# Performance work log

Hardware: AMD Instinct MI355X
Metric: run time of the kernel (lower is better)

## Reference

```python
import jax, jax.numpy as jnp
import numpy as np

NUM_TEAMS = 200000
EMBED_DIM = 16
NUM_EDGES = 3200000
BATCH = 500000
EPS_NORM = 1e-12  # F.normalize clamp
EPS_SOFTMAX = 1e-16  # PyG edge-softmax denom eps
NEG_SLOPE = 0.01  # LeakyReLU default


def setup_inputs() -> dict:
    key = jax.random.key(0)
    ks = jax.random.split(key, 12)
    inp = {}
    inp["embed"] = jax.random.normal(ks[0], (NUM_TEAMS, EMBED_DIM), dtype=jnp.float32)
    inp["beta"] = jnp.ones((2,), dtype=jnp.float32)  # one learnable scalar per AGNNConv
    # torch Linear init ~ U(-1/sqrt(fan_in), 1/sqrt(fan_in)); stored as [in, out]
    def lin(k, fi, fo):
        b = 1.0 / np.sqrt(fi)
        k1, k2 = jax.random.split(k)
        return (jax.random.uniform(k1, (fi, fo), jnp.float32, -b, b),
                jax.random.uniform(k2, (fo,), jnp.float32, -b, b))
    inp["lin0_w"], inp["lin0_b"] = lin(ks[1], 2 * EMBED_DIM, 6)
    inp["lin1_w"], inp["lin1_b"] = lin(ks[2], 6, 16)
    inp["lin2_w"], inp["lin2_b"] = lin(ks[3], 16, 3)
    inp["edge_index"] = jax.random.randint(ks[4], (2, NUM_EDGES), 0, NUM_TEAMS, dtype=jnp.int64)
    inp["home"] = jax.random.randint(ks[5], (BATCH,), 0, NUM_TEAMS, dtype=jnp.int64)
    inp["away"] = jax.random.randint(ks[6], (BATCH,), 0, NUM_TEAMS, dtype=jnp.int64)
    return inp


def _agnn_conv(x, beta, src, dst, n):
    # x: [N, D]; messages flow src(j) -> dst(i); scatter-softmax over edges per dst
    xn = x / jnp.maximum(jnp.linalg.norm(x, axis=-1, keepdims=True), EPS_NORM)
    alpha = beta * jnp.sum(xn[src] * xn[dst], axis=-1)          # [E]
    m = jax.ops.segment_max(alpha, dst, num_segments=n)          # [N]
    a = jnp.exp(alpha - m[dst])                                   # [E]
    denom = jax.ops.segment_sum(a, dst, num_segments=n)          # [N]
    a = a / (denom[dst] + EPS_SOFTMAX)
    return jax.ops.segment_sum(a[:, None] * x[src], dst, num_segments=n)  # [N, D]


def _forward(embed, beta, lin0_w, lin0_b, lin1_w, lin1_b, lin2_w, lin2_b,
             src, dst, home, away):
    n = embed.shape[0]
    act = lambda v: jax.nn.leaky_relu(v, NEG_SLOPE)
    x = embed  # embedding of arange(n_teams) == the table itself
    x = act(_agnn_conv(x, beta[0], src, dst, n))
    x = act(_agnn_conv(x, beta[1], src, dst, n))
    h = jnp.concatenate([x[home], x[away]], axis=-1)  # [B, 2D]
    h = act(h @ lin0_w + lin0_b)
    h = act(h @ lin1_w + lin1_b)
    h = act(h @ lin2_w + lin2_b)
    return jax.nn.log_softmax(h, axis=0).reshape(-1, 3)  # LogSoftmax(dim=0), faithful


def reference(embed, beta, lin0_w, lin0_b, lin1_w, lin1_b, lin2_w, lin2_b,
              edge_index, home, away):
    n = embed.shape[0]
    # AGNNConv default: remove then add self-loops
    loops = jnp.arange(n, dtype=edge_index.dtype)
    mask = edge_index[0] != edge_index[1]
    safe = jnp.where(mask, edge_index[1], edge_index[0])  # self-loop-out non-loop edges
    src = jnp.concatenate([edge_index[0], loops])
    dst = jnp.concatenate([jnp.where(mask, edge_index[1], edge_index[0]), loops])
    # masked self-loops in original list become src==dst duplicates of the appended
    # self-loops only if random collision; to faithfully *remove* them we redirect
    # removed edges onto the node's own appended self-loop (alpha identical for
    # src==dst), which changes only duplicate self-loop counts with prob ~1/N.
    return _forward(embed, beta, lin0_w, lin0_b, lin1_w, lin1_b, lin2_w, lin2_b,
                    src, dst, home, away)
```

## Files before the change

kernel.cpp:

```cpp
#include <hip/hip_runtime.h>
#include <hip/hip_fp16.h>
#include <math.h>

#define TPB 256
#define NPB 512
#define NPB_SHIFT 9
#define EPB 8192
#define EPW 16
#define BCAP 12288

typedef float v2f __attribute__((ext_vector_type(2)));

__device__ __forceinline__ float leaky_relu(float v) { return v > 0.0f ? v : 0.01f * v; }

__device__ __forceinline__ float dot4(float4 a, float4 b) {
    return a.x * b.x + a.y * b.y + a.z * b.z + a.w * b.w;
}
__device__ __forceinline__ float4 f4_scale(float4 a, float s) {
    return make_float4(a.x * s, a.y * s, a.z * s, a.w * s);
}
__device__ __forceinline__ float4 f4_acc(float4 a, float w, float4 y) {
    return make_float4(fmaf(w, y.x, a.x), fmaf(w, y.y, a.y),
                       fmaf(w, y.z, a.z), fmaf(w, y.w, a.w));
}
__device__ __forceinline__ float4 f4_add_shfl(float4 v, int d) {
    return make_float4(v.x + __shfl_xor(v.x, d, 64), v.y + __shfl_xor(v.y, d, 64),
                       v.z + __shfl_xor(v.z, d, 64), v.w + __shfl_xor(v.w, d, 64));
}
__device__ __forceinline__ float4 leaky4(float4 v) {
    return make_float4(leaky_relu(v.x), leaky_relu(v.y), leaky_relu(v.z), leaky_relu(v.w));
}

__device__ __forceinline__ float4 dec4(unsigned w) {
    v2f lo = __builtin_amdgcn_cvt_pk_f32_fp8((int)w, false);
    v2f hi = __builtin_amdgcn_cvt_pk_f32_fp8((int)w, true);
    return make_float4(lo.x, lo.y, hi.x, hi.y);
}
__device__ __forceinline__ unsigned enc4(float4 v) {
    int r = __builtin_amdgcn_cvt_pk_fp8_f32(v.x, v.y, 0, false);
    r = __builtin_amdgcn_cvt_pk_fp8_f32(v.z, v.w, r, true);
    return (unsigned)r;
}

__device__ __forceinline__ void store_h4(__half* row, int l, float4 v) {
    union { float2 f; __half h[4]; } u;
    u.h[0] = __float2half(v.x); u.h[1] = __float2half(v.y);
    u.h[2] = __float2half(v.z); u.h[3] = __float2half(v.w);
    ((float2*)row)[l] = u.f;
}

__device__ __forceinline__ int wave_incl_scan(int v, int lane) {
#pragma unroll
    for (int off = 1; off < 64; off <<= 1) {
        int u = __shfl_up(v, off, 64);
        if (lane >= off) v += u;
    }
    return v;
}

__global__ void k_binA(const int* __restrict__ src, const int* __restrict__ dst,
                       unsigned* __restrict__ bdata, int* __restrict__ cbase,
                       int* __restrict__ ccnt, int E, int K,
                       const float* __restrict__ x, uint4* __restrict__ xq,
                       int N) {
    __shared__ int hist[512];
    __shared__ unsigned lcol[EPB];
    __shared__ int wsum[8];
    int t = threadIdx.x;
    int lane = t & 63, wv = t >> 6;
    int c = blockIdx.x;
    int e0 = c * EPB;
    int e1 = min(e0 + EPB, E);
    int tot = e1 - e0;
    hist[t] = 0;
    __syncthreads();
    int myd[EPW], mys[EPW];
    if (tot == EPB) {
        const int4* d4 = (const int4*)(dst + e0);
        const int4* s4 = (const int4*)(src + e0);
#pragma unroll
        for (int k = 0; k < 4; ++k) {
            int4 dd = d4[t + k * 512];
            int4 ss = s4[t + k * 512];
            myd[4 * k + 0] = dd.x; myd[4 * k + 1] = dd.y;
            myd[4 * k + 2] = dd.z; myd[4 * k + 3] = dd.w;
            mys[4 * k + 0] = ss.x; mys[4 * k + 1] = ss.y;
            mys[4 * k + 2] = ss.z; mys[4 * k + 3] = ss.w;
            atomicAdd(&hist[dd.x >> NPB_SHIFT], 1);
            atomicAdd(&hist[dd.y >> NPB_SHIFT], 1);
            atomicAdd(&hist[dd.z >> NPB_SHIFT], 1);
            atomicAdd(&hist[dd.w >> NPB_SHIFT], 1);
        }
    } else {
#pragma unroll
        for (int k = 0; k < EPW; ++k) {
            int e = e0 + t + k * 512;
            int d = (e < e1) ? dst[e] : -1;
            mys[k] = (e < e1) ? src[e] : 0;
            myd[k] = d;
            if (d >= 0) atomicAdd(&hist[d >> NPB_SHIFT], 1);
        }
    }
    __syncthreads();
    int v = hist[t];
    int inc = wave_incl_scan(v, lane);
    if (lane == 63) wsum[wv] = inc;
    __syncthreads();
    if (t == 0) {
        int acc = 0;
#pragma unroll
        for (int k = 0; k < 8; ++k) { int xv = wsum[k]; wsum[k] = acc; acc += xv; }
    }
    __syncthreads();
    int excl = inc + wsum[wv] - v;
    if (t < K) {
        cbase[(size_t)c * K + t] = excl;
        ccnt[(size_t)c * K + t] = v;
    }
    __syncthreads();
    hist[t] = excl;
    __syncthreads();
    if (tot == EPB) {
#pragma unroll
        for (int k = 0; k < EPW; ++k) {
            int d = myd[k];
            int p = atomicAdd(&hist[d >> NPB_SHIFT], 1);
            lcol[p] = ((unsigned)(d & (NPB - 1)) << 18) | (unsigned)mys[k];
        }
    } else {
#pragma unroll
        for (int k = 0; k < EPW; ++k) {
            int d = myd[k];
            if (d >= 0) {
                int p = atomicAdd(&hist[d >> NPB_SHIFT], 1);
                lcol[p] = ((unsigned)(d & (NPB - 1)) << 18) | (unsigned)mys[k];
            }
        }
    }
    __syncthreads();
    unsigned* outp = bdata + (size_t)c * EPB;
    for (int i = t; i < tot; i += 512) outp[i] = lcol[i];
    int i = c * 512 + t;
    if (i < N) {
        const float4* xp = (const float4*)(x + (size_t)i * 16);
        float4 a = xp[0], b = xp[1], cc = xp[2], d = xp[3];
        xq[i] = make_uint4(enc4(a), enc4(b), enc4(cc), enc4(d));
    }
}

__global__ void k_binB(const unsigned* __restrict__ bdata, const int* __restrict__ cbase,
                       const int* __restrict__ ccnt,
                       int2* __restrict__ rng,
                       int* __restrict__ col, int N, int NC, int K) {
    __shared__ int cb[512];
    __shared__ int cc[512];
    __shared__ int ldeg[NPB];
    __shared__ int wsum[8];
    int b = blockIdx.x, t = threadIdx.x;
    int lane = t & 63, wv = t >> 6;
    int n0 = b << NPB_SHIFT;
    int nn = min(NPB, N - n0);
    cb[t] = (t < NC) ? cbase[(size_t)t * K + b] : 0;
    cc[t] = (t < NC) ? ccnt[(size_t)t * K + b] : 0;
    ldeg[t] = 0;
    __syncthreads();
    int mycnt = (t < NC) ? cc[t] : 0;
    const unsigned* myp = bdata + (size_t)t * EPB + cb[t];
    for (int k = 0; k < mycnt; ++k) {
        unsigned e = myp[k];
        atomicAdd(&ldeg[e >> 18], 1);
    }
    __syncthreads();
    int dv = ldeg[t];
    int inc = wave_incl_scan(dv, lane);
    if (lane == 63) wsum[wv] = inc;
    __syncthreads();
    if (t == 0) {
        int acc = 0;
#pragma unroll
        for (int k = 0; k < 8; ++k) { int xv = wsum[k]; wsum[k] = acc; acc += xv; }
    }
    __syncthreads();
    int excl = inc + wsum[wv] - dv;
    int gb = b * BCAP;
    if (t < nn) {
        rng[n0 + t] = make_int2(gb + excl, gb + excl + dv);
    }
    __syncthreads();
    ldeg[t] = excl;
    __syncthreads();
    for (int k = 0; k < mycnt; ++k) {
        unsigned e = myp[k];
        int pos = atomicAdd(&ldeg[e >> 18], 1);
        col[gb + pos] = (int)(e & 0x3FFFFu);
    }
}

__global__ void k_agnn(const uint4* __restrict__ xq,
                       const int2* __restrict__ rng,
                       const int* __restrict__ col,
                       const float* __restrict__ beta_ptr, int beta_idx,
                       void* __restrict__ out, int n, int fp8_out) {
    int t = threadIdx.x;
    int l = t & 7;
    int i = blockIdx.x * (512 / 8) + (t >> 3);
    if (i >= n) return;
    float bet = beta_ptr[beta_idx];
    uint4 rowi = xq[i];
    float4 x0 = dec4(rowi.x), x1 = dec4(rowi.y), x2 = dec4(rowi.z), x3 = dec4(rowi.w);
    float sqi = dot4(x0, x0) + dot4(x1, x1) + dot4(x2, x2) + dot4(x3, x3);
    float inv_ni = rsqrtf(fmaxf(sqi, 1e-24f));
    float bi = bet * inv_ni;
    float4 q0 = f4_scale(x0, bi), q1 = f4_scale(x1, bi),
           q2 = f4_scale(x2, bi), q3 = f4_scale(x3, bi);
    float s;
    float4 a0, a1, a2, a3;
    if (l == 0) {
        float w = __expf(bet);
        s = w;
        a0 = f4_scale(x0, w); a1 = f4_scale(x1, w);
        a2 = f4_scale(x2, w); a3 = f4_scale(x3, w);
    } else {
        s = 0.0f;
        a0 = a1 = a2 = a3 = make_float4(0.f, 0.f, 0.f, 0.f);
    }
    int2 se = rng[i];
    int e1 = se.y;
    int last = max(e1 - 1, 0);
    int e = se.x + l;
    int j0 = min(max(col[min(e, last)], 0), n - 1);
    uint4 rA = xq[j0];
    int j1 = min(max(col[min(e + 8, last)], 0), n - 1);
    uint4 rB = xq[j1];
    for (; e < e1; e += 8) {
        int j2 = min(max(col[min(e + 16, last)], 0), n - 1);
        uint4 rC = xq[j2];
        float4 y0 = dec4(rA.x), y1 = dec4(rA.y), y2 = dec4(rA.z), y3 = dec4(rA.w);
        float sq = dot4(y0, y0) + dot4(y1, y1) + dot4(y2, y2) + dot4(y3, y3);
        float inv_n = rsqrtf(fmaxf(sq, 1e-24f));
        float d = (dot4(y0, q0) + dot4(y1, q1) + dot4(y2, q2) + dot4(y3, q3)) * inv_n;
        float w = __expf(d);
        s += w;
        a0 = f4_acc(a0, w, y0);
        a1 = f4_acc(a1, w, y1);
        a2 = f4_acc(a2, w, y2);
        a3 = f4_acc(a3, w, y3);
        rA = rB; rB = rC;
    }
#pragma unroll
    for (int d_ = 1; d_ < 8; d_ <<= 1) {
        s += __shfl_xor(s, d_, 64);
        a0 = f4_add_shfl(a0, d_);
        a1 = f4_add_shfl(a1, d_);
        a2 = f4_add_shfl(a2, d_);
        a3 = f4_add_shfl(a3, d_);
    }
    float inv = 1.0f / (s + 1e-16f);
    float4 o0 = leaky4(f4_scale(a0, inv));
    float4 o1 = leaky4(f4_scale(a1, inv));
    float4 o2 = leaky4(f4_scale(a2, inv));
    float4 o3 = leaky4(f4_scale(a3, inv));
    if (l < 4) {
        float4 oq = (l == 0) ? o0 : (l == 1) ? o1 : (l == 2) ? o2 : o3;
        if (fp8_out) {
            ((unsigned*)((uint4*)out + i))[l] = enc4(oq);
        } else {
            store_h4((__half*)out + (size_t)i * 16, l, oq);
        }
    }
}

__global__ void k_mlp(const __half* __restrict__ x, const int* __restrict__ home,
                      const int* __restrict__ away,
                      const float* __restrict__ w0, const float* __restrict__ b0,
                      const float* __restrict__ w1, const float* __restrict__ b1,
                      const float* __restrict__ w2, const float* __restrict__ b2,
                      float* __restrict__ z, float* __restrict__ bmax,
                      float* __restrict__ bsum, int nb) {
    __shared__ float sw0[192], sw1[96], sw2[48], sb0[6], sb1[16], sb2[3];
    __shared__ float rmax[4][3];
    __shared__ float rsum[4][3];
    int t = threadIdx.x;
    if (t < 192) sw0[t] = w0[t];
    if (t < 96)  sw1[t] = w1[t];
    if (t < 48)  sw2[t] = w2[t];
    if (t < 6)   sb0[t] = b0[t];
    if (t < 16)  sb1[t] = b1[t];
    if (t < 3)   sb2[t] = b2[t];
    __syncthreads();
    int i = blockIdx.x * blockDim.x + t;
    bool act = i < nb;
    float z0 = -3.4e38f, z1 = -3.4e38f, z2 = -3.4e38f;
    if (act) {
        float h[32];
        const uint4* hr = (const uint4*)(x + (size_t)home[i] * 16);
        const uint4* ar = (const uint4*)(x + (size_t)away[i] * 16);
        uint4 hv0 = hr[0], hv1 = hr[1];
        uint4 av0 = ar[0], av1 = ar[1];
        union { uint4 u; __half2 h2[4]; } cv;
#pragma unroll
        for (int q = 0; q < 4; ++q) {
            cv.u = (q == 0) ? hv0 : (q == 1) ? hv1 : (q == 2) ? av0 : av1;
#pragma unroll
            for (int k = 0; k < 4; ++k) {
                float2 f = __half22float2(cv.h2[k]);
                h[q * 8 + 2 * k + 0] = f.x;
                h[q * 8 + 2 * k + 1] = f.y;
            }
        }
        float t0[6];
#pragma unroll
        for (int o = 0; o < 6; ++o) {
            float acc = sb0[o];
#pragma unroll
            for (int k = 0; k < 32; ++k) acc = fmaf(h[k], sw0[k * 6 + o], acc);
            t0[o] = leaky_relu(acc);
        }
        float t1[16];
#pragma unroll
        for (int o = 0; o < 16; ++o) {
            float acc = sb1[o];
#pragma unroll
            for (int k = 0; k < 6; ++k) acc = fmaf(t0[k], sw1[k * 16 + o], acc);
            t1[o] = leaky_relu(acc);
        }
        float zz[3];
#pragma unroll
        for (int o = 0; o < 3; ++o) {
            float acc = sb2[o];
#pragma unroll
            for (int k = 0; k < 16; ++k) acc = fmaf(t1[k], sw2[k * 3 + o], acc);
            zz[o] = leaky_relu(acc);
            z[(size_t)i * 3 + o] = zz[o];
        }
        z0 = zz[0]; z1 = zz[1]; z2 = zz[2];
    }
    float w0_ = z0, w1_ = z1, w2_ = z2;
#pragma unroll
    for (int off = 32; off > 0; off >>= 1) {
        w0_ = fmaxf(w0_, __shfl_down(w0_, off));
        w1_ = fmaxf(w1_, __shfl_down(w1_, off));
        w2_ = fmaxf(w2_, __shfl_down(w2_, off));
    }
    int wid = t >> 6;
    if ((t & 63) == 0) { rmax[wid][0] = w0_; rmax[wid][1] = w1_; rmax[wid][2] = w2_; }
    __syncthreads();
    float M0 = fmaxf(fmaxf(rmax[0][0], rmax[1][0]), fmaxf(rmax[2][0], rmax[3][0]));
    float M1 = fmaxf(fmaxf(rmax[0][1], rmax[1][1]), fmaxf(rmax[2][1], rmax[3][1]));
    float M2 = fmaxf(fmaxf(rmax[0][2], rmax[1][2]), fmaxf(rmax[2][2], rmax[3][2]));
    float e0 = act ? __expf(z0 - M0) : 0.0f;
    float e1 = act ? __expf(z1 - M1) : 0.0f;
    float e2 = act ? __expf(z2 - M2) : 0.0f;
#pragma unroll
    for (int off = 32; off > 0; off >>= 1) {
        e0 += __shfl_down(e0, off);
        e1 += __shfl_down(e1, off);
        e2 += __shfl_down(e2, off);
    }
    if ((t & 63) == 0) { rsum[wid][0] = e0; rsum[wid][1] = e1; rsum[wid][2] = e2; }
    __syncthreads();
    if (t == 0) {
        float S0 = rsum[0][0] + rsum[1][0] + rsum[2][0] + rsum[3][0];
        float S1 = rsum[0][1] + rsum[1][1] + rsum[2][1] + rsum[3][1];
        float S2 = rsum[0][2] + rsum[1][2] + rsum[2][2] + rsum[3][2];
        bmax[blockIdx.x * 3 + 0] = M0; bmax[blockIdx.x * 3 + 1] = M1; bmax[blockIdx.x * 3 + 2] = M2;
        bsum[blockIdx.x * 3 + 0] = S0; bsum[blockIdx.x * 3 + 1] = S1; bsum[blockIdx.x * 3 + 2] = S2;
    }
}

__device__ __forceinline__ float pick3(int c, float L0, float L1, float L2) {
    return c == 0 ? L0 : (c == 1 ? L1 : L2);
}

__global__ void k_final(const float4* __restrict__ z4,
                        const float* __restrict__ bmax, const float* __restrict__ bsum,
                        int nblk, float4* __restrict__ out4, int n4) {
    __shared__ float lm[4][3];
    __shared__ float ls[4][3];
    __shared__ float Lsh[3];
    int t = threadIdx.x;
    float M0 = -3.4e38f, M1 = -3.4e38f, M2 = -3.4e38f;
    float S0 = 0.f, S1 = 0.f, S2 = 0.f;
    for (int b = t; b < nblk; b += 256) {
        float m0 = bmax[b * 3 + 0], s0 = bsum[b * 3 + 0];
        float n0 = fmaxf(M0, m0); S0 = S0 * __expf(M0 - n0) + s0 * __expf(m0 - n0); M0 = n0;
        float m1 = bmax[b * 3 + 1], s1 = bsum[b * 3 + 1];
        float n1 = fmaxf(M1, m1); S1 = S1 * __expf(M1 - n1) + s1 * __expf(m1 - n1); M1 = n1;
        float m2 = bmax[b * 3 + 2], s2 = bsum[b * 3 + 2];
        float n2 = fmaxf(M2, m2); S2 = S2 * __expf(M2 - n2) + s2 * __expf(m2 - n2); M2 = n2;
    }
#pragma unroll
    for (int off = 32; off > 0; off >>= 1) {
        float mo, so, nm;
        mo = __shfl_down(M0, off); so = __shfl_down(S0, off);
        nm = fmaxf(M0, mo); S0 = S0 * __expf(M0 - nm) + so * __expf(mo - nm); M0 = nm;
        mo = __shfl_down(M1, off); so = __shfl_down(S1, off);
        nm = fmaxf(M1, mo); S1 = S1 * __expf(M1 - nm) + so * __expf(mo - nm); M1 = nm;
        mo = __shfl_down(M2, off); so = __shfl_down(S2, off);
        nm = fmaxf(M2, mo); S2 = S2 * __expf(M2 - nm) + so * __expf(mo - nm); M2 = nm;
    }
    int wid = t >> 6;
    if ((t & 63) == 0) {
        lm[wid][0] = M0; lm[wid][1] = M1; lm[wid][2] = M2;
        ls[wid][0] = S0; ls[wid][1] = S1; ls[wid][2] = S2;
    }
    __syncthreads();
    if (t == 0) {
        for (int w = 1; w < 4; ++w) {
            float nm;
            nm = fmaxf(M0, lm[w][0]); S0 = S0 * __expf(M0 - nm) + ls[w][0] * __expf(lm[w][0] - nm); M0 = nm;
            nm = fmaxf(M1, lm[w][1]); S1 = S1 * __expf(M1 - nm) + ls[w][1] * __expf(lm[w][1] - nm); M1 = nm;
            nm = fmaxf(M2, lm[w][2]); S2 = S2 * __expf(M2 - nm) + ls[w][2] * __expf(lm[w][2] - nm); M2 = nm;
        }
        Lsh[0] = M0 + logf(S0);
        Lsh[1] = M1 + logf(S1);
        Lsh[2] = M2 + logf(S2);
    }
    __syncthreads();
    float L0 = Lsh[0], L1 = Lsh[1], L2 = Lsh[2];
    int i = blockIdx.x * blockDim.x + t;
    if (i >= n4) return;
    float4 v = z4[i];
    int c = i % 3;
    int c1 = (c + 1) % 3, c2 = (c + 2) % 3;
    out4[i] = make_float4(v.x - pick3(c, L0, L1, L2),
                          v.y - pick3(c1, L0, L1, L2),
                          v.z - pick3(c2, L0, L1, L2),
                          v.w - pick3(c, L0, L1, L2));
}

extern "C" void kernel_launch(void* const* d_in, const int* in_sizes, int n_in,
                              void* d_out, int out_size, void* d_ws, size_t ws_size,
                              hipStream_t stream) {
    const float* embed = (const float*)d_in[0];
    const float* beta  = (const float*)d_in[1];
    const float* w0 = (const float*)d_in[2];
    const float* b0 = (const float*)d_in[3];
    const float* w1 = (const float*)d_in[4];
    const float* b1 = (const float*)d_in[5];
    const float* w2 = (const float*)d_in[6];
    const float* b2 = (const float*)d_in[7];
    const int* eidx = (const int*)d_in[8];
    const int* home = (const int*)d_in[9];
    const int* away = (const int*)d_in[10];

    const int N = in_sizes[0] / 16;
    const int E = in_sizes[8] / 2;
    const int B = in_sizes[9];
    const int* esrc = eidx;
    const int* edst = eidx + E;
    const int K = (N + NPB - 1) >> NPB_SHIFT;
    const int NC = (E + EPB - 1) / EPB;

    char* ws = (char*)d_ws;
    size_t off = 0;
    auto alloc = [&](size_t bytes) -> char* {
        off = (off + 255) & ~(size_t)255;
        char* p = ws + off;
        off += bytes;
        return p;
    };
    size_t bdata_bytes = (size_t)NC * EPB * 4;
    size_t alias_bytes = (((size_t)N * 16 + 511) & ~(size_t)255) + (size_t)B * 3 * 4;
    char* U = alloc(bdata_bytes > alias_bytes ? bdata_bytes : alias_bytes);
    unsigned* bdata = (unsigned*)U;
    uint4* xq1  = (uint4*)U;
    float* zbuf = (float*)(U + (((size_t)N * 16 + 511) & ~(size_t)255));

    int2* rng    = (int2*)alloc((size_t)N * 8);
    int* colw    = (int*)alloc((size_t)K * BCAP * 4);
    int* cbase   = (int*)alloc((size_t)NC * K * 4);
    int* ccnt    = (int*)alloc((size_t)NC * K * 4);
    uint4* xq0   = (uint4*)alloc((size_t)N * 16);
    __half* xh2  = (__half*)alloc((size_t)N * 32);
    const int nblkB = (B + TPB - 1) / TPB;
    float* bmax  = (float*)alloc((size_t)nblkB * 3 * 4);
    float* bsum  = (float*)alloc((size_t)nblkB * 3 * 4);
    (void)ws_size; (void)n_in; (void)out_size;

    k_binA<<<NC, 512, 0, stream>>>(esrc, edst, bdata, cbase, ccnt, E, K,
                                   embed, xq0, N);
    k_binB<<<K, 512, 0, stream>>>(bdata, cbase, ccnt, rng, colw, N, NC, K);

    const int nblkN8 = (N + 63) / 64;
    k_agnn<<<nblkN8, 512, 0, stream>>>(xq0, rng, colw, beta, 0, xq1, N, 1);
    k_agnn<<<nblkN8, 512, 0, stream>>>(xq1, rng, colw, beta, 1, xh2, N, 0);

    k_mlp<<<nblkB, TPB, 0, stream>>>(xh2, home, away, w0, b0, w1, b1, w2, b2,
                                     zbuf, bmax, bsum, B);
    const int n4 = (B * 3) / 4;
    k_final<<<(n4 + TPB - 1) / TPB, TPB, 0, stream>>>((const float4*)zbuf, bmax, bsum,
                                                      nblkB, (float4*)d_out, n4);
}
```

Measured before the change: 214.3 us.

## Scatter edge chunks directly into per-bucket windows via global atomic offsets

The first binning pass now reserves space in each destination bucket's final window with a global atomicAdd on a per-bucket counter. It writes its locally sorted edges straight there, finding each edge's bucket by binary search over the exclusive scan. The second pass loads its whole bucket window into LDS and sorts in place, which replaces the strided per-chunk reads and the cbase/ccnt tables. This removes one intermediate buffer round trip and the poorly coalesced per-thread sequential reads, at the cost of a memset, global atomics, nondeterministic edge order within buckets, and a 48KB LDS tile in binB that limits occupancy.

After: 216.9 us. About the same (+1.2%).

```diff
diff --git a/kernel.cpp b/kernel.cpp
--- a/kernel.cpp
+++ b/kernel.cpp
@@ -59,11 +59,13 @@
 }
 
 __global__ void k_binA(const int* __restrict__ src, const int* __restrict__ dst,
-                       unsigned* __restrict__ bdata, int* __restrict__ cbase,
-                       int* __restrict__ ccnt, int E, int K,
+                       unsigned* __restrict__ colw, int* __restrict__ gcnt,
+                       int E, int K,
                        const float* __restrict__ x, uint4* __restrict__ xq,
                        int N) {
     __shared__ int hist[512];
+    __shared__ int exs[512];
+    __shared__ int goff[512];
     __shared__ unsigned lcol[EPB];
     __shared__ int wsum[8];
     int t = threadIdx.x;
@@ -113,9 +115,10 @@
     }
     __syncthreads();
     int excl = inc + wsum[wv] - v;
+    exs[t] = excl;
     if (t < K) {
-        cbase[(size_t)c * K + t] = excl;
-        ccnt[(size_t)c * K + t] = v;
+        int g = (v > 0) ? atomicAdd(&gcnt[t], v) : 0;
+        goff[t] = g - excl;
     }
     __syncthreads();
     hist[t] = excl;
@@ -138,8 +141,15 @@
         }
     }
     __syncthreads();
-    unsigned* outp = bdata + (size_t)c * EPB;
-    for (int i = t; i < tot; i += 512) outp[i] = lcol[i];
+    for (int i = t; i < tot; i += 512) {
+        int b = 0;
+#pragma unroll
+        for (int s = 256; s > 0; s >>= 1) {
+            int nb = b + s;
+            if (nb < 512 && exs[nb] <= i) b = nb;
+        }
+        colw[(size_t)b * BCAP + goff[b] + i] = lcol[i];
+    }
     int i = c * 512 + t;
     if (i < N) {
         const float4* xp = (const float4*)(x + (size_t)i * 16);
@@ -148,28 +158,21 @@
     }
 }
 
-__global__ void k_binB(const unsigned* __restrict__ bdata, const int* __restrict__ cbase,
-                       const int* __restrict__ ccnt,
-                       int2* __restrict__ rng,
-                       int* __restrict__ col, int N, int NC, int K) {
-    __shared__ int cb[512];
-    __shared__ int cc[512];
+__global__ void k_binB(unsigned* __restrict__ colw, const int* __restrict__ gcnt,
+                       int2* __restrict__ rng, int N) {
+    __shared__ unsigned tags[BCAP];
     __shared__ int ldeg[NPB];
     __shared__ int wsum[8];
     int b = blockIdx.x, t = threadIdx.x;
     int lane = t & 63, wv = t >> 6;
     int n0 = b << NPB_SHIFT;
     int nn = min(NPB, N - n0);
-    cb[t] = (t < NC) ? cbase[(size_t)t * K + b] : 0;
-    cc[t] = (t < NC) ? ccnt[(size_t)t * K + b] : 0;
+    int cnt = gcnt[b];
+    unsigned* win = colw + (size_t)b * BCAP;
+    for (int i = t; i < cnt; i += 512) tags[i] = win[i];
     ldeg[t] = 0;
     __syncthreads();
-    int mycnt = (t < NC) ? cc[t] : 0;
-    const unsigned* myp = bdata + (size_t)t * EPB + cb[t];
-    for (int k = 0; k < mycnt; ++k) {
-        unsigned e = myp[k];
-        atomicAdd(&ldeg[e >> 18], 1);
-    }
+    for (int i = t; i < cnt; i += 512) atomicAdd(&ldeg[tags[i] >> 18], 1);
     __syncthreads();
     int dv = ldeg[t];
     int inc = wave_incl_scan(dv, lane);
@@ -189,10 +192,10 @@
     __syncthreads();
     ldeg[t] = excl;
     __syncthreads();
-    for (int k = 0; k < mycnt; ++k) {
-        unsigned e = myp[k];
-        int pos = atomicAdd(&ldeg[e >> 18], 1);
-        col[gb + pos] = (int)(e & 0x3FFFFu);
+    for (int i = t; i < cnt; i += 512) {
+        unsigned tg = tags[i];
+        int pos = atomicAdd(&ldeg[tg >> 18], 1);
+        win[pos] = tg & 0x3FFFFu;
     }
 }
 
@@ -460,31 +463,25 @@
         off += bytes;
         return p;
     };
-    size_t bdata_bytes = (size_t)NC * EPB * 4;
-    size_t alias_bytes = (((size_t)N * 16 + 511) & ~(size_t)255) + (size_t)B * 3 * 4;
-    char* U = alloc(bdata_bytes > alias_bytes ? bdata_bytes : alias_bytes);
-    unsigned* bdata = (unsigned*)U;
-    uint4* xq1  = (uint4*)U;
-    float* zbuf = (float*)(U + (((size_t)N * 16 + 511) & ~(size_t)255));
-
+    unsigned* colw = (unsigned*)alloc((size_t)K * BCAP * 4);
+    int* gcnt    = (int*)alloc((size_t)K * 4);
     int2* rng    = (int2*)alloc((size_t)N * 8);
-    int* colw    = (int*)alloc((size_t)K * BCAP * 4);
-    int* cbase   = (int*)alloc((size_t)NC * K * 4);
-    int* ccnt    = (int*)alloc((size_t)NC * K * 4);
     uint4* xq0   = (uint4*)alloc((size_t)N * 16);
+    uint4* xq1   = (uint4*)alloc((size_t)N * 16);
+    float* zbuf  = (float*)alloc((size_t)B * 3 * 4);
     __half* xh2  = (__half*)alloc((size_t)N * 32);
     const int nblkB = (B + TPB - 1) / TPB;
     float* bmax  = (float*)alloc((size_t)nblkB * 3 * 4);
     float* bsum  = (float*)alloc((size_t)nblkB * 3 * 4);
     (void)ws_size; (void)n_in; (void)out_size;
 
-    k_binA<<<NC, 512, 0, stream>>>(esrc, edst, bdata, cbase, ccnt, E, K,
-                                   embed, xq0, N);
-    k_binB<<<K, 512, 0, stream>>>(bdata, cbase, ccnt, rng, colw, N, NC, K);
+    hipMemsetAsync(gcnt, 0, (size_t)K * 4, stream);
+    k_binA<<<NC, 512, 0, stream>>>(esrc, edst, colw, gcnt, E, K, embed, xq0, N);
+    k_binB<<<K, 512, 0, stream>>>(colw, gcnt, rng, N);
 
     const int nblkN8 = (N + 63) / 64;
-    k_agnn<<<nblkN8, 512, 0, stream>>>(xq0, rng, colw, beta, 0, xq1, N, 1);
-    k_agnn<<<nblkN8, 512, 0, stream>>>(xq1, rng, colw, beta, 1, xh2, N, 0);
+    k_agnn<<<nblkN8, 512, 0, stream>>>(xq0, rng, (const int*)colw, beta, 0, xq1, N, 1);
+    k_agnn<<<nblkN8, 512, 0, stream>>>(xq1, rng, (const int*)colw, beta, 1, xh2, N, 0);
 
     k_mlp<<<nblkB, TPB, 0, stream>>>(xh2, home, away, w0, b0, w1, b1, w2, b2,
                                      zbuf, bmax, bsum, B);
```

## Fuse all stages into one persistent cooperative kernel with grid syncs

Applied to the files above, without the earlier changes.

Replaces the six separate kernel launches (binning, CSR build, two AGNN layers, MLP, final log-softmax) with one cooperative persistent kernel. Stages are separated by grid-wide barriers, and each stage loops over its work items by block stride. Shared memory is reused through a union. The aim is to remove launch gaps and tail effects between small kernels. In exchange, the grid is capped, grid-sync overhead is added, and occupancy limits apply (launch bounds 512x4 with about 34 KB of shared memory per block). The old multi-kernel path stays as a fallback if the cooperative launch fails.

Measured after the change: 433.2 us. 2.02x slower.

```diff
diff --git a/kernel.cpp b/kernel.cpp
--- a/kernel.cpp
+++ b/kernel.cpp
@@ -1,6 +1,9 @@
 #include <hip/hip_runtime.h>
 #include <hip/hip_fp16.h>
+#include <hip/hip_cooperative_groups.h>
 #include <math.h>
+
+namespace cg = cooperative_groups;
 
 #define TPB 256
 #define NPB 512
@@ -8,6 +11,8 @@
 #define EPB 8192
 #define EPW 16
 #define BCAP 12288
+#define FUSED_TPB 512
+#define MAXGRID 1280
 
 typedef float v2f __attribute__((ext_vector_type(2)));
 
@@ -58,21 +63,25 @@
     return v;
 }
 
-__global__ void k_binA(const int* __restrict__ src, const int* __restrict__ dst,
-                       unsigned* __restrict__ bdata, int* __restrict__ cbase,
-                       int* __restrict__ ccnt, int E, int K,
-                       const float* __restrict__ x, uint4* __restrict__ xq,
-                       int N) {
-    __shared__ int hist[512];
-    __shared__ unsigned lcol[EPB];
-    __shared__ int wsum[8];
+struct SA { int hist[512]; int wsum[8]; unsigned lcol[EPB]; };
+struct SB { int cb[512]; int cc[512]; int ldeg[NPB]; int wsum[8]; };
+struct SM { float sw0[192], sw1[96], sw2[48], sb0[6], sb1[16], sb2[3];
+            float rmax[8][3], rsum[8][3]; };
+struct SF { float lm[8][3], ls[8][3], Lsh[3]; };
+union SU { SA a; SB b; SM m; SF f; };
+
+
+__device__ void binA_dev(int c, const int* __restrict__ src, const int* __restrict__ dst,
+                         unsigned* __restrict__ bdata, int* __restrict__ cbase,
+                         int* __restrict__ ccnt, int E, int K,
+                         const float* __restrict__ x, uint4* __restrict__ xq,
+                         int N, SA& s) {
     int t = threadIdx.x;
     int lane = t & 63, wv = t >> 6;
-    int c = blockIdx.x;
     int e0 = c * EPB;
     int e1 = min(e0 + EPB, E);
     int tot = e1 - e0;
-    hist[t] = 0;
+    s.hist[t] = 0;
     __syncthreads();
     int myd[EPW], mys[EPW];
     if (tot == EPB) {
@@ -86,10 +95,10 @@
             myd[4 * k + 2] = dd.z; myd[4 * k + 3] = dd.w;
             mys[4 * k + 0] = ss.x; mys[4 * k + 1] = ss.y;
             mys[4 * k + 2] = ss.z; mys[4 * k + 3] = ss.w;
-            atomicAdd(&hist[dd.x >> NPB_SHIFT], 1);
-            atomicAdd(&hist[dd.y >> NPB_SHIFT], 1);
-            atomicAdd(&hist[dd.z >> NPB_SHIFT], 1);
-            atomicAdd(&hist[dd.w >> NPB_SHIFT], 1);
+            atomicAdd(&s.hist[dd.x >> NPB_SHIFT], 1);
+            atomicAdd(&s.hist[dd.y >> NPB_SHIFT], 1);
+            atomicAdd(&s.hist[dd.z >> NPB_SHIFT], 1);
+            atomicAdd(&s.hist[dd.w >> NPB_SHIFT], 1);
         }
     } else {
 #pragma unroll
@@ -98,114 +107,106 @@
             int d = (e < e1) ? dst[e] : -1;
             mys[k] = (e < e1) ? src[e] : 0;
             myd[k] = d;
-            if (d >= 0) atomicAdd(&hist[d >> NPB_SHIFT], 1);
-        }
-    }
-    __syncthreads();
-    int v = hist[t];
+            if (d >= 0) atomicAdd(&s.hist[d >> NPB_SHIFT], 1);
+        }
+    }
+    __syncthreads();
+    int v = s.hist[t];
     int inc = wave_incl_scan(v, lane);
-    if (lane == 63) wsum[wv] = inc;
+    if (lane == 63) s.wsum[wv] = inc;
     __syncthreads();
     if (t == 0) {
         int acc = 0;
 #pragma unroll
-        for (int k = 0; k < 8; ++k) { int xv = wsum[k]; wsum[k] = acc; acc += xv; }
-    }
-    __syncthreads();
-    int excl = inc + wsum[wv] - v;
+        for (int k = 0; k < 8; ++k) { int xv = s.wsum[k]; s.wsum[k] = acc; acc += xv; }
+    }
+    __syncthreads();
+    int excl = inc + s.wsum[wv] - v;
     if (t < K) {
         cbase[(size_t)c * K + t] = excl;
         ccnt[(size_t)c * K + t] = v;
     }
     __syncthreads();
-    hist[t] = excl;
+    s.hist[t] = excl;
     __syncthreads();
     if (tot == EPB) {
 #pragma unroll
         for (int k = 0; k < EPW; ++k) {
             int d = myd[k];
-            int p = atomicAdd(&hist[d >> NPB_SHIFT], 1);
-            lcol[p] = ((unsigned)(d & (NPB - 1)) << 18) | (unsigned)mys[k];
+            int p = atomicAdd(&s.hist[d >> NPB_SHIFT], 1);
+            s.lcol[p] = ((unsigned)(d & (NPB - 1)) << 18) | (unsigned)mys[k];
         }
     } else {
 #pragma unroll
         for (int k = 0; k < EPW; ++k) {
             int d = myd[k];
             if (d >= 0) {
-                int p = atomicAdd(&hist[d >> NPB_SHIFT], 1);
-                lcol[p] = ((unsigned)(d & (NPB - 1)) << 18) | (unsigned)mys[k];
+                int p = atomicAdd(&s.hist[d >> NPB_SHIFT], 1);
+                s.lcol[p] = ((unsigned)(d & (NPB - 1)) << 18) | (unsigned)mys[k];
             }
         }
     }
     __syncthreads();
     unsigned* outp = bdata + (size_t)c * EPB;
-    for (int i = t; i < tot; i += 512) outp[i] = lcol[i];
+    for (int i = t; i < tot; i += 512) outp[i] = s.lcol[i];
     int i = c * 512 + t;
     if (i < N) {
         const float4* xp = (const float4*)(x + (size_t)i * 16);
         float4 a = xp[0], b = xp[1], cc = xp[2], d = xp[3];
         xq[i] = make_uint4(enc4(a), enc4(b), enc4(cc), enc4(d));
     }
-}
-
-__global__ void k_binB(const unsigned* __restrict__ bdata, const int* __restrict__ cbase,
-                       const int* __restrict__ ccnt,
-                       int2* __restrict__ rng,
-                       int* __restrict__ col, int N, int NC, int K) {
-    __shared__ int cb[512];
-    __shared__ int cc[512];
-    __shared__ int ldeg[NPB];
-    __shared__ int wsum[8];
-    int b = blockIdx.x, t = threadIdx.x;
+    __syncthreads();
+}
+
+__device__ void binB_dev(int b, const unsigned* __restrict__ bdata,
+                         const int* __restrict__ cbase, const int* __restrict__ ccnt,
+                         int2* __restrict__ rng, int* __restrict__ col,
+                         int N, int NC, int K, SB& s) {
+    int t = threadIdx.x;
     int lane = t & 63, wv = t >> 6;
     int n0 = b << NPB_SHIFT;
     int nn = min(NPB, N - n0);
-    cb[t] = (t < NC) ? cbase[(size_t)t * K + b] : 0;
-    cc[t] = (t < NC) ? ccnt[(size_t)t * K + b] : 0;
-    ldeg[t] = 0;
-    __syncthreads();
-    int mycnt = (t < NC) ? cc[t] : 0;
-    const unsigned* myp = bdata + (size_t)t * EPB + cb[t];
+    s.cb[t] = (t < NC) ? cbase[(size_t)t * K + b] : 0;
+    s.cc[t] = (t < NC) ? ccnt[(size_t)t * K + b] : 0;
+    s.ldeg[t] = 0;
+    __syncthreads();
+    int mycnt = (t < NC) ? s.cc[t] : 0;
+    const unsigned* myp = bdata + (size_t)t * EPB + s.cb[t];
     for (int k = 0; k < mycnt; ++k) {
         unsigned e = myp[k];
-        atomicAdd(&ldeg[e >> 18], 1);
-    }
-    __syncthreads();
-    int dv = ldeg[t];
+        atomicAdd(&s.ldeg[e >> 18], 1);
+    }
+    __syncthreads();
+    int dv = s.ldeg[t];
     int inc = wave_incl_scan(dv, lane);
-    if (lane == 63) wsum[wv] = inc;
+    if (lane == 63) s.wsum[wv] = inc;
     __syncthreads();
     if (t == 0) {
         int acc = 0;
 #pragma unroll
-        for (int k = 0; k < 8; ++k) { int xv = wsum[k]; wsum[k] = acc; acc += xv; }
-    }
-    __syncthreads();
-    int excl = inc + wsum[wv] - dv;
+        for (int k = 0; k < 8; ++k) { int xv = s.wsum[k]; s.wsum[k] = acc; acc += xv; }
+    }
+    __syncthreads();
+    int excl = inc + s.wsum[wv] - dv;
     int gb = b * BCAP;
     if (t < nn) {
         rng[n0 + t] = make_int2(gb + excl, gb + excl + dv);
     }
     __syncthreads();
-    ldeg[t] = excl;
+    s.ldeg[t] = excl;
     __syncthreads();
     for (int k = 0; k < mycnt; ++k) {
         unsigned e = myp[k];
-        int pos = atomicAdd(&ldeg[e >> 18], 1);
+        int pos = atomicAdd(&s.ldeg[e >> 18], 1);
         col[gb + pos] = (int)(e & 0x3FFFFu);
     }
-}
-
-__global__ void k_agnn(const uint4* __restrict__ xq,
-                       const int2* __restrict__ rng,
-                       const int* __restrict__ col,
-                       const float* __restrict__ beta_ptr, int beta_idx,
-                       void* __restrict__ out, int n, int fp8_out) {
-    int t = threadIdx.x;
-    int l = t & 7;
-    int i = blockIdx.x * (512 / 8) + (t >> 3);
+    __syncthreads();
+}
+
+__device__ void agnn_dev(int i, int l, const uint4* __restrict__ xq,
+                         const int2* __restrict__ rng, const int* __restrict__ col,
+                         float bet, void* __restrict__ out, int n, int fp8_out) {
     if (i >= n) return;
-    float bet = beta_ptr[beta_idx];
     uint4 rowi = xq[i];
     float4 x0 = dec4(rowi.x), x1 = dec4(rowi.y), x2 = dec4(rowi.z), x3 = dec4(rowi.w);
     float sqi = dot4(x0, x0) + dot4(x1, x1) + dot4(x2, x2) + dot4(x3, x3);
@@ -270,69 +271,258 @@
     }
 }
 
-__global__ void k_mlp(const __half* __restrict__ x, const int* __restrict__ home,
-                      const int* __restrict__ away,
-                      const float* __restrict__ w0, const float* __restrict__ b0,
-                      const float* __restrict__ w1, const float* __restrict__ b1,
-                      const float* __restrict__ w2, const float* __restrict__ b2,
-                      float* __restrict__ z, float* __restrict__ bmax,
-                      float* __restrict__ bsum, int nb) {
-    __shared__ float sw0[192], sw1[96], sw2[48], sb0[6], sb1[16], sb2[3];
-    __shared__ float rmax[4][3];
-    __shared__ float rsum[4][3];
+__device__ __forceinline__ void mlp_row_dev(int i, const __half* __restrict__ x,
+                                            const int* __restrict__ home,
+                                            const int* __restrict__ away,
+                                            const SM& m, float* __restrict__ z,
+                                            float zz[3]) {
+    float h[32];
+    const uint4* hr = (const uint4*)(x + (size_t)home[i] * 16);
+    const uint4* ar = (const uint4*)(x + (size_t)away[i] * 16);
+    uint4 hv0 = hr[0], hv1 = hr[1];
+    uint4 av0 = ar[0], av1 = ar[1];
+    union { uint4 u; __half2 h2[4]; } cv;
+#pragma unroll
+    for (int q = 0; q < 4; ++q) {
+        cv.u = (q == 0) ? hv0 : (q == 1) ? hv1 : (q == 2) ? av0 : av1;
+#pragma unroll
+        for (int k = 0; k < 4; ++k) {
+            float2 f = __half22float2(cv.h2[k]);
+            h[q * 8 + 2 * k + 0] = f.x;
+            h[q * 8 + 2 * k + 1] = f.y;
+        }
+    }
+    float t0[6];
+#pragma unroll
+    for (int o = 0; o < 6; ++o) {
+        float acc = m.sb0[o];
+#pragma unroll
+        for (int k = 0; k < 32; ++k) acc = fmaf(h[k], m.sw0[k * 6 + o], acc);
+        t0[o] = leaky_relu(acc);
+    }
+    float t1[16];
+#pragma unroll
+    for (int o = 0; o < 16; ++o) {
+        float acc = m.sb1[o];
+#pragma unroll
+        for (int k = 0; k < 6; ++k) acc = fmaf(t0[k], m.sw1[k * 16 + o], acc);
+        t1[o] = leaky_relu(acc);
+    }
+#pragma unroll
+    for (int o = 0; o < 3; ++o) {
+        float acc = m.sb2[o];
+#pragma unroll
+        for (int k = 0; k < 16; ++k) acc = fmaf(t1[k], m.sw2[k * 3 + o], acc);
+        zz[o] = leaky_relu(acc);
+        z[(size_t)i * 3 + o] = zz[o];
+    }
+}
+
+__device__ __forceinline__ float pick3(int c, float L0, float L1, float L2) {
+    return c == 0 ? L0 : (c == 1 ? L1 : L2);
+}
+
+__global__ void __launch_bounds__(FUSED_TPB, 4)
+k_fused(const int* esrc, const int* edst,
+        unsigned* bdata, int* cbase, int* ccnt,
+        int E, int K, int NC,
+        const float* embed, uint4* xq0, uint4* xq1, int N, int nVB,
+        int2* rng, int* colw, const float* beta, __half* xh2,
+        const int* home, const int* away,
+        const float* w0, const float* b0, const float* w1, const float* b1,
+        const float* w2, const float* b2,
+        float* zbuf, float* bmax, float* bsum, int Bn, int nChunkM,
+        float4* out4, int n4) {
+    __shared__ SU su;
+    cg::grid_group grid = cg::this_grid();
+    int bid = blockIdx.x, nb = gridDim.x;
     int t = threadIdx.x;
-    if (t < 192) sw0[t] = w0[t];
-    if (t < 96)  sw1[t] = w1[t];
-    if (t < 48)  sw2[t] = w2[t];
-    if (t < 6)   sb0[t] = b0[t];
-    if (t < 16)  sb1[t] = b1[t];
-    if (t < 3)   sb2[t] = b2[t];
+    int wid = t >> 6;
+
+    for (int c = bid; c < NC; c += nb)
+        binA_dev(c, esrc, edst, bdata, cbase, ccnt, E, K, embed, xq0, N, su.a);
+    grid.sync();
+    for (int b = bid; b < K; b += nb)
+        binB_dev(b, bdata, cbase, ccnt, rng, colw, N, NC, K, su.b);
+    grid.sync();
+    {
+        float bet = beta[0];
+        int l = t & 7;
+        for (int vb = bid; vb < nVB; vb += nb)
+            agnn_dev(vb * 64 + (t >> 3), l, xq0, rng, colw, bet, xq1, N, 1);
+    }
+    grid.sync();
+    {
+        float bet = beta[1];
+        int l = t & 7;
+        for (int vb = bid; vb < nVB; vb += nb)
+            agnn_dev(vb * 64 + (t >> 3), l, xq1, rng, colw, bet, xh2, N, 0);
+    }
+    grid.sync();
+    {
+        SM& m = su.m;
+        if (t < 192) m.sw0[t] = w0[t];
+        if (t < 96)  m.sw1[t] = w1[t];
+        if (t < 48)  m.sw2[t] = w2[t];
+        if (t < 6)   m.sb0[t] = b0[t];
+        if (t < 16)  m.sb1[t] = b1[t];
+        if (t < 3)   m.sb2[t] = b2[t];
+        __syncthreads();
+        float rM0 = -3.4e38f, rM1 = -3.4e38f, rM2 = -3.4e38f;
+        float rS0 = 0.f, rS1 = 0.f, rS2 = 0.f;
+        for (int c = bid; c < nChunkM; c += nb) {
+            int i = c * FUSED_TPB + t;
+            bool act = i < Bn;
+            float z0 = -3.4e38f, z1 = -3.4e38f, z2 = -3.4e38f;
+            if (act) {
+                float zz[3];
+                mlp_row_dev(i, xh2, home, away, m, zbuf, zz);
+                z0 = zz[0]; z1 = zz[1]; z2 = zz[2];
+            }
+            float w0_ = z0, w1_ = z1, w2_ = z2;
+#pragma unroll
+            for (int off = 32; off > 0; off >>= 1) {
+                w0_ = fmaxf(w0_, __shfl_down(w0_, off));
+                w1_ = fmaxf(w1_, __shfl_down(w1_, off));
+                w2_ = fmaxf(w2_, __shfl_down(w2_, off));
+            }
+            if ((t & 63) == 0) { m.rmax[wid][0] = w0_; m.rmax[wid][1] = w1_; m.rmax[wid][2] = w2_; }
+            __syncthreads();
+            float M0 = m.rmax[0][0], M1 = m.rmax[0][1], M2 = m.rmax[0][2];
+#pragma unroll
+            for (int w = 1; w < 8; ++w) {
+                M0 = fmaxf(M0, m.rmax[w][0]);
+                M1 = fmaxf(M1, m.rmax[w][1]);
+                M2 = fmaxf(M2, m.rmax[w][2]);
+            }
+            float e0 = act ? __expf(z0 - M0) : 0.0f;
+            float e1 = act ? __expf(z1 - M1) : 0.0f;
+            float e2 = act ? __expf(z2 - M2) : 0.0f;
+#pragma unroll
+            for (int off = 32; off > 0; off >>= 1) {
+                e0 += __shfl_down(e0, off);
+                e1 += __shfl_down(e1, off);
+                e2 += __shfl_down(e2, off);
+            }
+            if ((t & 63) == 0) { m.rsum[wid][0] = e0; m.rsum[wid][1] = e1; m.rsum[wid][2] = e2; }
+            __syncthreads();
+            if (t == 0) {
+                float S0 = 0.f, S1 = 0.f, S2 = 0.f;
+#pragma unroll
+                for (int w = 0; w < 8; ++w) { S0 += m.rsum[w][0]; S1 += m.rsum[w][1]; S2 += m.rsum[w][2]; }
+                float nm;
+                nm = fmaxf(rM0, M0); rS0 = rS0 * __expf(rM0 - nm) + S0 * __expf(M0 - nm); rM0 = nm;
+                nm = fmaxf(rM1, M1); rS1 = rS1 * __expf(rM1 - nm) + S1 * __expf(M1 - nm); rM1 = nm;
+                nm = fmaxf(rM2, M2); rS2 = rS2 * __expf(rM2 - nm) + S2 * __expf(M2 - nm); rM2 = nm;
+            }
+            __syncthreads();
+        }
+        if (t == 0) {
+            bmax[bid * 3 + 0] = rM0; bmax[bid * 3 + 1] = rM1; bmax[bid * 3 + 2] = rM2;
+            bsum[bid * 3 + 0] = rS0; bsum[bid * 3 + 1] = rS1; bsum[bid * 3 + 2] = rS2;
+        }
+    }
+    grid.sync();
+    {
+        SF& f = su.f;
+        int nblk = nb;
+        float M0 = -3.4e38f, M1 = -3.4e38f, M2 = -3.4e38f;
+        float S0 = 0.f, S1 = 0.f, S2 = 0.f;
+        for (int b = t; b < nblk; b += FUSED_TPB) {
+            float m0 = bmax[b * 3 + 0], s0 = bsum[b * 3 + 0];
+            float n0 = fmaxf(M0, m0); S0 = S0 * __expf(M0 - n0) + s0 * __expf(m0 - n0); M0 = n0;
+            float m1 = bmax[b * 3 + 1], s1 = bsum[b * 3 + 1];
+            float n1 = fmaxf(M1, m1); S1 = S1 * __expf(M1 - n1) + s1 * __expf(m1 - n1); M1 = n1;
+            float m2 = bmax[b * 3 + 2], s2 = bsum[b * 3 + 2];
+            float n2 = fmaxf(M2, m2); S2 = S2 * __expf(M2 - n2) + s2 * __expf(m2 - n2); M2 = n2;
+        }
+#pragma unroll
+        for (int off = 32; off > 0; off >>= 1) {
+            float mo, so, nm;
+            mo = __shfl_down(M0, off); so = __shfl_down(S0, off);
+            nm = fmaxf(M0, mo); S0 = S0 * __expf(M0 - nm) + so * __expf(mo - nm); M0 = nm;
+            mo = __shfl_down(M1, off); so = __shfl_down(S1, off);
+            nm = fmaxf(M1, mo); S1 = S1 * __expf(M1 - nm) + so * __expf(mo - nm); M1 = nm;
+            mo = __shfl_down(M2, off); so = __shfl_down(S2, off);
+            nm = fmaxf(M2, mo); S2 = S2 * __expf(M2 - nm) + so * __expf(mo - nm); M2 = nm;
+        }
+        if ((t & 63) == 0) {
+            f.lm[wid][0] = M0; f.lm[wid][1] = M1; f.lm[wid][2] = M2;
+            f.ls[wid][0] = S0; f.ls[wid][1] = S1; f.ls[wid][2] = S2;
+        }
+        __syncthreads();
+        if (t == 0) {
+            for (int w = 1; w < 8; ++w) {
+                float nm;
+                nm = fmaxf(M0, f.lm[w][0]); S0 = S0 * __expf(M0 - nm) + f.ls[w][0] * __expf(f.lm[w][0] - nm); M0 = nm;
+                nm = fmaxf(M1, f.lm[w][1]); S1 = S1 * __expf(M1 - nm) + f.ls[w][1] * __expf(f.lm[w][1] - nm); M1 = nm;
+                nm = fmaxf(M2, f.lm[w][2]); S2 = S2 * __expf(M2 - nm) + f.ls[w][2] * __expf(f.lm[w][2] - nm); M2 = nm;
+            }
+            f.Lsh[0] = M0 + logf(S0);
+            f.Lsh[1] = M1 + logf(S1);
+            f.Lsh[2] = M2 + logf(S2);
+        }
+        __syncthreads();
+        float L0 = f.Lsh[0], L1 = f.Lsh[1], L2 = f.Lsh[2];
+        const float4* z4 = (const float4*)zbuf;
+        for (int i = bid * FUSED_TPB + t; i < n4; i += nb * FUSED_TPB) {
+            float4 v = z4[i];
+            int c = i % 3;
+            int c1 = (c + 1) % 3, c2 = (c + 2) % 3;
+            out4[i] = make_float4(v.x - pick3(c, L0, L1, L2),
+                                  v.y - pick3(c1, L0, L1, L2),
+                                  v.z - pick3(c2, L0, L1, L2),
+                                  v.w - pick3(c, L0, L1, L2));
+        }
+    }
+}
+
+
+__global__ void k_binA_s(const int* __restrict__ src, const int* __restrict__ dst,
+                         unsigned* __restrict__ bdata, int* __restrict__ cbase,
+                         int* __restrict__ ccnt, int E, int K,
+                         const float* __restrict__ x, uint4* __restrict__ xq, int N) {
+    __shared__ SA s;
+    binA_dev(blockIdx.x, src, dst, bdata, cbase, ccnt, E, K, x, xq, N, s);
+}
+
+__global__ void k_binB_s(const unsigned* __restrict__ bdata, const int* __restrict__ cbase,
+                         const int* __restrict__ ccnt, int2* __restrict__ rng,
+                         int* __restrict__ col, int N, int NC, int K) {
+    __shared__ SB s;
+    binB_dev(blockIdx.x, bdata, cbase, ccnt, rng, col, N, NC, K, s);
+}
+
+__global__ void k_agnn_s(const uint4* __restrict__ xq, const int2* __restrict__ rng,
+                         const int* __restrict__ col, const float* __restrict__ beta_ptr,
+                         int beta_idx, void* __restrict__ out, int n, int fp8_out) {
+    int t = threadIdx.x;
+    int i = blockIdx.x * (512 / 8) + (t >> 3);
+    agnn_dev(i, t & 7, xq, rng, col, beta_ptr[beta_idx], out, n, fp8_out);
+}
+
+__global__ void k_mlp_s(const __half* __restrict__ x, const int* __restrict__ home,
+                        const int* __restrict__ away,
+                        const float* __restrict__ w0, const float* __restrict__ b0,
+                        const float* __restrict__ w1, const float* __restrict__ b1,
+                        const float* __restrict__ w2, const float* __restrict__ b2,
+                        float* __restrict__ z, float* __restrict__ bmax,
+                        float* __restrict__ bsum, int nb) {
+    __shared__ SM m;
+    int t = threadIdx.x;
+    if (t < 192) m.sw0[t] = w0[t];
+    if (t < 96)  m.sw1[t] = w1[t];
+    if (t < 48)  m.sw2[t] = w2[t];
+    if (t < 6)   m.sb0[t] = b0[t];
+    if (t < 16)  m.sb1[t] = b1[t];
+    if (t < 3)   m.sb2[t] = b2[t];
     __syncthreads();
     int i = blockIdx.x * blockDim.x + t;
     bool act = i < nb;
     float z0 = -3.4e38f, z1 = -3.4e38f, z2 = -3.4e38f;
     if (act) {
-        float h[32];
-        const uint4* hr = (const uint4*)(x + (size_t)home[i] * 16);
-        const uint4* ar = (const uint4*)(x + (size_t)away[i] * 16);
-        uint4 hv0 = hr[0], hv1 = hr[1];
-        uint4 av0 = ar[0], av1 = ar[1];
-        union { uint4 u; __half2 h2[4]; } cv;
-#pragma unroll
-        for (int q = 0; q < 4; ++q) {
-            cv.u = (q == 0) ? hv0 : (q == 1) ? hv1 : (q == 2) ? av0 : av1;
-#pragma unroll
-            for (int k = 0; k < 4; ++k) {
-                float2 f = __half22float2(cv.h2[k]);
-                h[q * 8 + 2 * k + 0] = f.x;
-                h[q * 8 + 2 * k + 1] = f.y;
-            }
-        }
-        float t0[6];
-#pragma unroll
-        for (int o = 0; o < 6; ++o) {
-            float acc = sb0[o];
-#pragma unroll
-            for (int k = 0; k < 32; ++k) acc = fmaf(h[k], sw0[k * 6 + o], acc);
-            t0[o] = leaky_relu(acc);
-        }
-        float t1[16];
-#pragma unroll
-        for (int o = 0; o < 16; ++o) {
-            float acc = sb1[o];
-#pragma unroll
-            for (int k = 0; k < 6; ++k) acc = fmaf(t0[k], sw1[k * 16 + o], acc);
-            t1[o] = leaky_relu(acc);
-        }
         float zz[3];
-#pragma unroll
-        for (int o = 0; o < 3; ++o) {
-            float acc = sb2[o];
-#pragma unroll
-            for (int k = 0; k < 16; ++k) acc = fmaf(t1[k], sw2[k * 3 + o], acc);
-            zz[o] = leaky_relu(acc);
-            z[(size_t)i * 3 + o] = zz[o];
-        }
+        mlp_row_dev(i, x, home, away, m, z, zz);
         z0 = zz[0]; z1 = zz[1]; z2 = zz[2];
     }
     float w0_ = z0, w1_ = z1, w2_ = z2;
@@ -343,11 +533,11 @@
         w2_ = fmaxf(w2_, __shfl_down(w2_, off));
     }
     int wid = t >> 6;
-    if ((t & 63) == 0) { rmax[wid][0] = w0_; rmax[wid][1] = w1_; rmax[wid][2] = w2_; }
-    __syncthreads();
-    float M0 = fmaxf(fmaxf(rmax[0][0], rmax[1][0]), fmaxf(rmax[2][0], rmax[3][0]));
-    float M1 = fmaxf(fmaxf(rmax[0][1], rmax[1][1]), fmaxf(rmax[2][1], rmax[3][1]));
-    float M2 = fmaxf(fmaxf(rmax[0][2], rmax[1][2]), fmaxf(rmax[2][2], rmax[3][2]));
+    if ((t & 63) == 0) { m.rmax[wid][0] = w0_; m.rmax[wid][1] = w1_; m.rmax[wid][2] = w2_; }
+    __syncthreads();
+    float M0 = fmaxf(fmaxf(m.rmax[0][0], m.rmax[1][0]), fmaxf(m.rmax[2][0], m.rmax[3][0]));
+    float M1 = fmaxf(fmaxf(m.rmax[0][1], m.rmax[1][1]), fmaxf(m.rmax[2][1], m.rmax[3][1]));
+    float M2 = fmaxf(fmaxf(m.rmax[0][2], m.rmax[1][2]), fmaxf(m.rmax[2][2], m.rmax[3][2]));
     float e0 = act ? __expf(z0 - M0) : 0.0f;
     float e1 = act ? __expf(z1 - M1) : 0.0f;
     float e2 = act ? __expf(z2 - M2) : 0.0f;
@@ -357,27 +547,21 @@
         e1 += __shfl_down(e1, off);
         e2 += __shfl_down(e2, off);
     }
-    if ((t & 63) == 0) { rsum[wid][0] = e0; rsum[wid][1] = e1; rsum[wid][2] = e2; }
+    if ((t & 63) == 0) { m.rsum[wid][0] = e0; m.rsum[wid][1] = e1; m.rsum[wid][2] = e2; }
     __syncthreads();
     if (t == 0) {
-        float S0 = rsum[0][0] + rsum[1][0] + rsum[2][0] + rsum[3][0];
-        float S1 = rsum[0][1] + rsum[1][1] + rsum[2][1] + rsum[3][1];
-        float S2 = rsum[0][2] + rsum[1][2] + rsum[2][2] + rsum[3][2];
+        float S0 = m.rsum[0][0] + m.rsum[1][0] + m.rsum[2][0] + m.rsum[3][0];
+        float S1 = m.rsum[0][1] + m.rsum[1][1] + m.rsum[2][1] + m.rsum[3][1];
+        float S2 = m.rsum[0][2] + m.rsum[1][2] + m.rsum[2][2] + m.rsum[3][2];
         bmax[blockIdx.x * 3 + 0] = M0; bmax[blockIdx.x * 3 + 1] = M1; bmax[blockIdx.x * 3 + 2] = M2;
         bsum[blockIdx.x * 3 + 0] = S0; bsum[blockIdx.x * 3 + 1] = S1; bsum[blockIdx.x * 3 + 2] = S2;
     }
 }
 
-__device__ __forceinline__ float pick3(int c, float L0, float L1, float L2) {
-    return c == 0 ? L0 : (c == 1 ? L1 : L2);
-}
-
-__global__ void k_final(const float4* __restrict__ z4,
-                        const float* __restrict__ bmax, const float* __restrict__ bsum,
-                        int nblk, float4* __restrict__ out4, int n4) {
-    __shared__ float lm[4][3];
-    __shared__ float ls[4][3];
-    __shared__ float Lsh[3];
+__global__ void k_final_s(const float4* __restrict__ z4,
+                          const float* __restrict__ bmax, const float* __restrict__ bsum,
+                          int nblk, float4* __restrict__ out4, int n4) {
+    __shared__ SF f;
     int t = threadIdx.x;
     float M0 = -3.4e38f, M1 = -3.4e38f, M2 = -3.4e38f;
     float S0 = 0.f, S1 = 0.f, S2 = 0.f;
@@ -401,23 +585,23 @@
     }
     int wid = t >> 6;
     if ((t & 63) == 0) {
-        lm[wid][0] = M0; lm[wid][1] = M1; lm[wid][2] = M2;
-        ls[wid][0] = S0; ls[wid][1] = S1; ls[wid][2] = S2;
+        f.lm[wid][0] = M0; f.lm[wid][1] = M1; f.lm[wid][2] = M2;
+        f.ls[wid][0] = S0; f.ls[wid][1] = S1; f.ls[wid][2] = S2;
     }
     __syncthreads();
     if (t == 0) {
         for (int w = 1; w < 4; ++w) {
             float nm;
-            nm = fmaxf(M0, lm[w][0]); S0 = S0 * __expf(M0 - nm) + ls[w][0] * __expf(lm[w][0] - nm); M0 = nm;
-            nm = fmaxf(M1, lm[w][1]); S1 = S1 * __expf(M1 - nm) + ls[w][1] * __expf(lm[w][1] - nm); M1 = nm;
-            nm = fmaxf(M2, lm[w][2]); S2 = S2 * __expf(M2 - nm) + ls[w][2] * __expf(lm[w][2] - nm); M2 = nm;
-        }
-        Lsh[0] = M0 + logf(S0);
-        Lsh[1] = M1 + logf(S1);
-        Lsh[2] = M2 + logf(S2);
-    }
-    __syncthreads();
-    float L0 = Lsh[0], L1 = Lsh[1], L2 = Lsh[2];
+            nm = fmaxf(M0, f.lm[w][0]); S0 = S0 * __expf(M0 - nm) + f.ls[w][0] * __expf(f.lm[w][0] - nm); M0 = nm;
+            nm = fmaxf(M1, f.lm[w][1]); S1 = S1 * __expf(M1 - nm) + f.ls[w][1] * __expf(f.lm[w][1] - nm); M1 = nm;
+            nm = fmaxf(M2, f.lm[w][2]); S2 = S2 * __expf(M2 - nm) + f.ls[w][2] * __expf(f.lm[w][2] - nm); M2 = nm;
+        }
+        f.Lsh[0] = M0 + logf(S0);
+        f.Lsh[1] = M1 + logf(S1);
+        f.Lsh[2] = M2 + logf(S2);
+    }
+    __syncthreads();
+    float L0 = f.Lsh[0], L1 = f.Lsh[1], L2 = f.Lsh[2];
     int i = blockIdx.x * blockDim.x + t;
     if (i >= n4) return;
     float4 v = z4[i];
@@ -444,13 +628,13 @@
     const int* home = (const int*)d_in[9];
     const int* away = (const int*)d_in[10];
 
-    const int N = in_sizes[0] / 16;
-    const int E = in_sizes[8] / 2;
-    const int B = in_sizes[9];
+    int N = in_sizes[0] / 16;
+    int E = in_sizes[8] / 2;
+    int B = in_sizes[9];
     const int* esrc = eidx;
     const int* edst = eidx + E;
-    const int K = (N + NPB - 1) >> NPB_SHIFT;
-    const int NC = (E + EPB - 1) / EPB;
+    int K = (N + NPB - 1) >> NPB_SHIFT;
+    int NC = (E + EPB - 1) / EPB;
 
     char* ws = (char*)d_ws;
     size_t off = 0;
@@ -474,21 +658,52 @@
     uint4* xq0   = (uint4*)alloc((size_t)N * 16);
     __half* xh2  = (__half*)alloc((size_t)N * 32);
     const int nblkB = (B + TPB - 1) / TPB;
-    float* bmax  = (float*)alloc((size_t)nblkB * 3 * 4);
-    float* bsum  = (float*)alloc((size_t)nblkB * 3 * 4);
+    int npart = nblkB > MAXGRID ? nblkB : MAXGRID;
+    float* bmax  = (float*)alloc((size_t)npart * 3 * 4);
+    float* bsum  = (float*)alloc((size_t)npart * 3 * 4);
     (void)ws_size; (void)n_in; (void)out_size;
 
-    k_binA<<<NC, 512, 0, stream>>>(esrc, edst, bdata, cbase, ccnt, E, K,
-                                   embed, xq0, N);
-    k_binB<<<K, 512, 0, stream>>>(bdata, cbase, ccnt, rng, colw, N, NC, K);
-
-    const int nblkN8 = (N + 63) / 64;
-    k_agnn<<<nblkN8, 512, 0, stream>>>(xq0, rng, colw, beta, 0, xq1, N, 1);
-    k_agnn<<<nblkN8, 512, 0, stream>>>(xq1, rng, colw, beta, 1, xh2, N, 0);
-
-    k_mlp<<<nblkB, TPB, 0, stream>>>(xh2, home, away, w0, b0, w1, b1, w2, b2,
-                                     zbuf, bmax, bsum, B);
-    const int n4 = (B * 3) / 4;
-    k_final<<<(n4 + TPB - 1) / TPB, TPB, 0, stream>>>((const float4*)zbuf, bmax, bsum,
-                                                      nblkB, (float4*)d_out, n4);
-}
+    int nVB = (N + 63) / 64;
+    int nChunkM = (B + FUSED_TPB - 1) / FUSED_TPB;
+    int n4 = (B * 3) / 4;
+    float4* out4 = (float4*)d_out;
+    __half* xh2p = xh2;
+
+    bool done = false;
+    int maxPerCU = 0;
+    hipError_t qerr = hipOccupancyMaxActiveBlocksPerMultiprocessor(
+        &maxPerCU, (const void*)k_fused, FUSED_TPB, 0);
+    if (qerr == hipSuccess && maxPerCU > 0) {
+        int grid = maxPerCU * 256;
+        if (grid > MAXGRID) grid = MAXGRID;
+        void* args[] = {
+            (void*)&esrc, (void*)&edst, (void*)&bdata, (void*)&cbase, (void*)&ccnt,
+            (void*)&E, (void*)&K, (void*)&NC,
+            (void*)&embed, (void*)&xq0, (void*)&xq1, (void*)&N, (void*)&nVB,
+            (void*)&rng, (void*)&colw, (void*)&beta, (void*)&xh2p,
+            (void*)&home, (void*)&away,
+            (void*)&w0, (void*)&b0, (void*)&w1, (void*)&b1, (void*)&w2, (void*)&b2,
+            (void*)&zbuf, (void*)&bmax, (void*)&bsum, (void*)&B, (void*)&nChunkM,
+            (void*)&out4, (void*)&n4
+        };
+        hipError_t lerr = hipLaunchCooperativeKernel((const void*)k_fused, dim3(grid),
+                                                     dim3(FUSED_TPB), args, 0, stream);
+        if (lerr == hipSuccess) done = true;
+        else (void)hipGetLastError();
+    } else {
+        (void)hipGetLastError();
+    }
+
+    if (!done) {
+        k_binA_s<<<NC, 512, 0, stream>>>(esrc, edst, bdata, cbase, ccnt, E, K,
+                                         embed, xq0, N);
+        k_binB_s<<<K, 512, 0, stream>>>(bdata, cbase, ccnt, rng, colw, N, NC, K);
+        const int nblkN8 = (N + 63) / 64;
+        k_agnn_s<<<nblkN8, 512, 0, stream>>>(xq0, rng, colw, beta, 0, xq1, N, 1);
+        k_agnn_s<<<nblkN8, 512, 0, stream>>>(xq1, rng, colw, beta, 1, xh2, N, 0);
+        k_mlp_s<<<nblkB, TPB, 0, stream>>>(xh2, home, away, w0, b0, w1, b1, w2, b2,
+                                           zbuf, bmax, bsum, B);
+        k_final_s<<<(n4 + TPB - 1) / TPB, TPB, 0, stream>>>((const float4*)zbuf, bmax,
+                                                            bsum, nblkB, out4, n4);
+    }
+}
```
